# Performance work log

Measured on AMD Instinct MI355X. Metric: run time of the kernel, lower is better.

Reference implementation:

```python
import jax, jax.numpy as jnp
import numpy as np

B = 524288  # batch size
H = 4      # hidden dim


def _gru(x, h, Wih, Whh, bih, bhh):
    """PyTorch GRUCell semantics. x: [..., in], h: [..., H]."""
    gi = x @ Wih.T + bih          # [..., 3H]
    gh = h @ Whh.T + bhh          # [..., 3H]
    ir, iz, inn = jnp.split(gi, 3, axis=-1)
    hr, hz, hn = jnp.split(gh, 3, axis=-1)
    r = jax.nn.sigmoid(ir + hr)
    z = jax.nn.sigmoid(iz + hz)
    n = jnp.tanh(inn + r * hn)
    return (1.0 - z) * n + z * h


def setup_inputs() -> dict:
    key = jax.random.key(0)
    ks = jax.random.split(key, 16)
    s = 0.1
    return {
        "x": jax.random.normal(ks[0], (B, 18), dtype=jnp.float32),
        # fc_j_init: Linear(2, 4)
        "Wj": jax.random.normal(ks[1], (H, 2), dtype=jnp.float32) * s,
        "bj": jax.random.normal(ks[2], (H,), dtype=jnp.float32) * s,
        # fc_m_init: Linear(4, 4)
        "Wm": jax.random.normal(ks[3], (H, H), dtype=jnp.float32) * s,
        "bm": jax.random.normal(ks[4], (H,), dtype=jnp.float32) * s,
        # rnn_j: GRUCell(8, 4) (input is cat of two neighbor states)
        "Wih_j": jax.random.normal(ks[5], (3 * H, 2 * H), dtype=jnp.float32) * s,
        "Whh_j": jax.random.normal(ks[6], (3 * H, H), dtype=jnp.float32) * s,
        "bih_j": jax.random.normal(ks[7], (3 * H,), dtype=jnp.float32) * s,
        "bhh_j": jax.random.normal(ks[8], (3 * H,), dtype=jnp.float32) * s,
        # rnn_m: GRUCell(4, 4)
        "Wih_m": jax.random.normal(ks[9], (3 * H, H), dtype=jnp.float32) * s,
        "Whh_m": jax.random.normal(ks[10], (3 * H, H), dtype=jnp.float32) * s,
        "bih_m": jax.random.normal(ks[11], (3 * H,), dtype=jnp.float32) * s,
        "bhh_m": jax.random.normal(ks[12], (3 * H,), dtype=jnp.float32) * s,
        # fc_act: Linear(4, 1)
        "Wa": jax.random.normal(ks[13], (1, H), dtype=jnp.float32) * s,
        "ba": jax.random.normal(ks[14], (1,), dtype=jnp.float32) * s,
    }


def reference(x, Wj, bj, Wm, bm, Wih_j, Whh_j, bih_j, bhh_j,
              Wih_m, Whh_m, bih_m, bhh_m, Wa, ba):
    obs = x[:, :4]                       # [B, 4]
    j = x[:, 4:11]                       # [B, 7]
    jd = x[:, 11:18]                     # [B, 7]
    jcat = jnp.stack([j, jd], axis=-1)   # [B, 7, 2] per-joint (angle, vel)

    hj = jcat @ Wj.T + bj                # [B, 7, 4] joint hidden states
    hm = obs @ Wm.T + bm                 # [B, 4]   master hidden state

    zero_pad = jnp.zeros_like(hj[:, :1])  # [B, 1, 4] (node 6 has no right neighbor)
    for _ in range(7):
        hm_new = _gru(hj[:, 0], hm, Wih_m, Whh_m, bih_m, bhh_m)
        # left neighbor of node 0 is the master; of node i is node i-1
        left = jnp.concatenate([hm[:, None], hj[:, :6]], axis=1)   # [B, 7, 4]
        right = jnp.concatenate([hj[:, 1:], zero_pad], axis=1)     # [B, 7, 4]
        inp = jnp.concatenate([left, right], axis=-1)              # [B, 7, 8]
        hj = _gru(inp, hj, Wih_j, Whh_j, bih_j, bhh_j)             # all 7 nodes at once
        hm = hm_new

    acts = hj @ Wa.T + ba                # [B, 7, 1]
    return acts
```

## Files before the change

### kernel.cpp

```cpp
#include <hip/hip_runtime.h>


typedef _Float16 half2v __attribute__((ext_vector_type(2)));

__device__ __forceinline__ float fexp2(float x) { return __builtin_amdgcn_exp2f(x); }
__device__ __forceinline__ float frcp(float x)  { return __builtin_amdgcn_rcpf(x); }
__device__ __forceinline__ float fdot2(half2v a, half2v b, float c) {
    return __builtin_amdgcn_fdot2(a, b, c, false);
}
__device__ __forceinline__ half2v pkh(float a, float b) {
    return half2v{(_Float16)a, (_Float16)b};
}
__device__ __forceinline__ unsigned pku(float a, float b) {
    union { unsigned u; half2v h; } z; z.h = pkh(a, b); return z.u;
}
__device__ __forceinline__ half2v ldw(const unsigned* p, int i) {
    union { unsigned u; half2v h; } z; z.u = p[i]; return z.h;
}

#define U_PJRZ 0
#define U_PJNLR 48
#define U_PJNH 64
#define U_PMRZ 72
#define U_PMNI 104
#define U_PMNH 112
#define F_BRZJ 120
#define F_BINJ 128
#define F_BHNJ 132
#define F_BRZM 136
#define F_BINM 144
#define F_BHNM 148
#define F_WJ   152
#define F_BJ   160
#define F_WM   164
#define F_BM   180
#define F_WA   184
#define F_BA   188
#define W_TOT2 189

__global__ void pack_weights2(
    const float* __restrict__ Wj,    const float* __restrict__ bj,
    const float* __restrict__ Wm,    const float* __restrict__ bm,
    const float* __restrict__ Wih_j, const float* __restrict__ Whh_j,
    const float* __restrict__ bih_j, const float* __restrict__ bhh_j,
    const float* __restrict__ Wih_m, const float* __restrict__ Whh_m,
    const float* __restrict__ bih_m, const float* __restrict__ bhh_m,
    const float* __restrict__ Wa,    const float* __restrict__ ba,
    void* __restrict__ wsv)
{
    unsigned* wu = (unsigned*)wsv;
    float*    wf = (float*)wsv;
    int t = threadIdx.x;
    const float SN = -1.44269504088896f;
    const float ST =  2.88539008177793f;
    if (t < 48) {
        int g = t / 6, p = t % 6; float a, b;
        if (p < 4) { a = Wih_j[g*8 + 2*p];     b = Wih_j[g*8 + 2*p + 1]; }
        else       { a = Whh_j[g*4 + 2*(p-4)]; b = Whh_j[g*4 + 2*(p-4) + 1]; }
        wu[t] = pku(a * SN, b * SN);
    } else if (t < 64) {
        int i = t - 48, u = i / 4, p = i % 4;
        wu[t] = pku(Wih_j[(8+u)*8 + 2*p] * ST, Wih_j[(8+u)*8 + 2*p + 1] * ST);
    } else if (t < 72) {
        int i = t - 64, u = i / 2, p = i % 2;
        wu[t] = pku(Whh_j[(8+u)*4 + 2*p] * ST, Whh_j[(8+u)*4 + 2*p + 1] * ST);
    } else if (t < 104) {
        int i = t - 72, g = i / 4, p = i % 4; float a, b;
        if (p < 2) { a = Wih_m[g*4 + 2*p];     b = Wih_m[g*4 + 2*p + 1]; }
        else       { a = Whh_m[g*4 + 2*(p-2)]; b = Whh_m[g*4 + 2*(p-2) + 1]; }
        wu[t] = pku(a * SN, b * SN);
    } else if (t < 112) {
        int i = t - 104, u = i / 2, p = i % 2;
        wu[t] = pku(Wih_m[(8+u)*4 + 2*p] * ST, Wih_m[(8+u)*4 + 2*p + 1] * ST);
    } else if (t < 120) {
        int i = t - 112, u = i / 2, p = i % 2;
        wu[t] = pku(Whh_m[(8+u)*4 + 2*p] * ST, Whh_m[(8+u)*4 + 2*p + 1] * ST);
    } else if (t < 128) { wf[t] = (bih_j[t-120] + bhh_j[t-120]) * SN; }
    else if (t < 132)   { wf[t] = bih_j[8 + t - 128] * ST; }
    else if (t < 136)   { wf[t] = bhh_j[8 + t - 132] * ST; }
    else if (t < 144)   { wf[t] = (bih_m[t-136] + bhh_m[t-136]) * SN; }
    else if (t < 148)   { wf[t] = bih_m[8 + t - 144] * ST; }
    else if (t < 152)   { wf[t] = bhh_m[8 + t - 148] * ST; }
    else if (t < 160)   { wf[t] = Wj[t - 152]; }
    else if (t < 164)   { wf[t] = bj[t - 160]; }
    else if (t < 180)   { wf[t] = Wm[t - 164]; }
    else if (t < 184)   { wf[t] = bm[t - 180]; }
    else if (t < 188)   { wf[t] = Wa[t - 184]; }
    else if (t == 188)  { wf[t] = ba[0]; }
}

__global__ __launch_bounds__(256)
__attribute__((amdgpu_waves_per_eu(4, 4)))
void aggreg_policy_dot2(
    const float* __restrict__ x, const void* __restrict__ wsv,
    float* __restrict__ out, int nrows)
{
    const unsigned* WU = (const unsigned*)wsv;
    const float*    WF = (const float*)wsv;
    int b = blockIdx.x * blockDim.x + threadIdx.x;
    if (b >= nrows) return;

    const float2* xr2 = (const float2*)(x + (long)b * 18);
    float xin[18];
    #pragma unroll
    for (int i = 0; i < 9; ++i) { float2 v = xr2[i]; xin[2*i] = v.x; xin[2*i+1] = v.y; }

    float hj[7][4], hm[4];
    half2v pj[7][2], pm[2];

    #pragma unroll
    for (int k = 0; k < 7; ++k) {
        #pragma unroll
        for (int u = 0; u < 4; ++u)
            hj[k][u] = fmaf(WF[F_WJ + u*2], xin[4 + k],
                       fmaf(WF[F_WJ + u*2 + 1], xin[11 + k], WF[F_BJ + u]));
        pj[k][0] = pkh(hj[k][0], hj[k][1]);
        pj[k][1] = pkh(hj[k][2], hj[k][3]);
    }
    #pragma unroll
    for (int u = 0; u < 4; ++u) {
        float a = WF[F_BM + u];
        #pragma unroll
        for (int v = 0; v < 4; ++v) a = fmaf(WF[F_WM + u*4 + v], xin[v], a);
        hm[u] = a;
    }
    pm[0] = pkh(hm[0], hm[1]);
    pm[1] = pkh(hm[2], hm[3]);

    #pragma unroll 1
    for (int it = 0; it < 7; ++it) {
        float hmn[4]; half2v pmn[2];
        {
            float pre[8], inn[4], hn[4];
            #pragma unroll
            for (int g = 0; g < 8; ++g) {
                float a = WF[F_BRZM + g];
                a = fdot2(pj[0][0], ldw(WU, U_PMRZ + g*4 + 0), a);
                a = fdot2(pj[0][1], ldw(WU, U_PMRZ + g*4 + 1), a);
                a = fdot2(pm[0],    ldw(WU, U_PMRZ + g*4 + 2), a);
                a = fdot2(pm[1],    ldw(WU, U_PMRZ + g*4 + 3), a);
                pre[g] = a;
            }
            #pragma unroll
            for (int u = 0; u < 4; ++u) {
                float a = WF[F_BINM + u];
                a = fdot2(pj[0][0], ldw(WU, U_PMNI + u*2 + 0), a);
                a = fdot2(pj[0][1], ldw(WU, U_PMNI + u*2 + 1), a);
                inn[u] = a;
                float c = WF[F_BHNM + u];
                c = fdot2(pm[0], ldw(WU, U_PMNH + u*2 + 0), c);
                c = fdot2(pm[1], ldw(WU, U_PMNH + u*2 + 1), c);
                hn[u] = c;
            }
            #pragma unroll
            for (int u = 0; u < 4; ++u) {
                float r = frcp(1.0f + fexp2(pre[u]));
                float z = frcp(1.0f + fexp2(pre[4 + u]));
                float narg = fmaf(r, hn[u], inn[u]);
                float n = fmaf(-2.0f, frcp(1.0f + fexp2(narg)), 1.0f);
                hmn[u] = fmaf(z, hm[u] - n, n);
            }
            pmn[0] = pkh(hmn[0], hmn[1]);
            pmn[1] = pkh(hmn[2], hmn[3]);
        }

        float op[4]; half2v opp[2];
        #pragma unroll
        for (int k = 0; k < 7; ++k) {
            half2v L0 = (k == 0) ? pm[0] : opp[0];
            half2v L1 = (k == 0) ? pm[1] : opp[1];
            half2v H0 = pj[k][0], H1 = pj[k][1];
            float pre[8], inn[4], hn[4];
            #pragma unroll
            for (int g = 0; g < 8; ++g) {
                float a = WF[F_BRZJ + g];
                a = fdot2(L0, ldw(WU, U_PJRZ + g*6 + 0), a);
                a = fdot2(L1, ldw(WU, U_PJRZ + g*6 + 1), a);
                if (k != 6) {
                    a = fdot2(pj[k+1][0], ldw(WU, U_PJRZ + g*6 + 2), a);
                    a = fdot2(pj[k+1][1], ldw(WU, U_PJRZ + g*6 + 3), a);
                }
                a = fdot2(H0, ldw(WU, U_PJRZ + g*6 + 4), a);
                a = fdot2(H1, ldw(WU, U_PJRZ + g*6 + 5), a);
                pre[g] = a;
            }
            #pragma unroll
            for (int u = 0; u < 4; ++u) {
                float a = WF[F_BINJ + u];
                a = fdot2(L0, ldw(WU, U_PJNLR + u*4 + 0), a);
                a = fdot2(L1, ldw(WU, U_PJNLR + u*4 + 1), a);
                if (k != 6) {
                    a = fdot2(pj[k+1][0], ldw(WU, U_PJNLR + u*4 + 2), a);
                    a = fdot2(pj[k+1][1], ldw(WU, U_PJNLR + u*4 + 3), a);
                }
                inn[u] = a;
                float c = WF[F_BHNJ + u];
                c = fdot2(H0, ldw(WU, U_PJNH + u*2 + 0), c);
                c = fdot2(H1, ldw(WU, U_PJNH + u*2 + 1), c);
                hn[u] = c;
            }
            float nh[4];
            #pragma unroll
            for (int u = 0; u < 4; ++u) {
                float r = frcp(1.0f + fexp2(pre[u]));
                float z = frcp(1.0f + fexp2(pre[4 + u]));
                float narg = fmaf(r, hn[u], inn[u]);
                float n = fmaf(-2.0f, frcp(1.0f + fexp2(narg)), 1.0f);
                nh[u] = fmaf(z, hj[k][u] - n, n);
            }
            #pragma unroll
            for (int u = 0; u < 4; ++u) { op[u] = hj[k][u]; hj[k][u] = nh[u]; }
            opp[0] = pj[k][0]; opp[1] = pj[k][1];
            pj[k][0] = pkh(nh[0], nh[1]);
            pj[k][1] = pkh(nh[2], nh[3]);
        }

        #pragma unroll
        for (int u = 0; u < 4; ++u) hm[u] = hmn[u];
        pm[0] = pmn[0]; pm[1] = pmn[1];
    }

    float* orow = out + (long)b * 7;
    #pragma unroll
    for (int k = 0; k < 7; ++k) {
        float a = WF[F_BA];
        #pragma unroll
        for (int u = 0; u < 4; ++u) a = fmaf(WF[F_WA + u], hj[k][u], a);
        orow[k] = a;
    }
}

__device__ __forceinline__ float sigmoid_f(float x) {
    return frcp(1.0f + fexp2(-1.44269504088896f * x));
}
__device__ __forceinline__ float tanh_f(float x) {
    float e = fexp2(2.88539008177793f * x);
    return 1.0f - 2.0f * frcp(1.0f + e);
}

__global__ __launch_bounds__(256) void aggreg_policy_fallback(
    const float* __restrict__ x,
    const float* __restrict__ Wj,    const float* __restrict__ bj,
    const float* __restrict__ Wm,    const float* __restrict__ bm,
    const float* __restrict__ Wih_j, const float* __restrict__ Whh_j,
    const float* __restrict__ bih_j, const float* __restrict__ bhh_j,
    const float* __restrict__ Wih_m, const float* __restrict__ Whh_m,
    const float* __restrict__ bih_m, const float* __restrict__ bhh_m,
    const float* __restrict__ Wa,    const float* __restrict__ ba,
    float* __restrict__ out, int nrows)
{
    int b = blockIdx.x * blockDim.x + threadIdx.x;
    if (b >= nrows) return;
    const float* xr = x + (long)b * 18;
    float obs[4], jv[7], jd[7];
    #pragma unroll
    for (int i = 0; i < 4; ++i) obs[i] = xr[i];
    #pragma unroll
    for (int i = 0; i < 7; ++i) jv[i] = xr[4 + i];
    #pragma unroll
    for (int i = 0; i < 7; ++i) jd[i] = xr[11 + i];
    float hj[7][4], hm[4];
    #pragma unroll
    for (int k = 0; k < 7; ++k)
        #pragma unroll
        for (int u = 0; u < 4; ++u)
            hj[k][u] = fmaf(Wj[u*2], jv[k], fmaf(Wj[u*2+1], jd[k], bj[u]));
    #pragma unroll
    for (int u = 0; u < 4; ++u) {
        float a = bm[u];
        #pragma unroll
        for (int v = 0; v < 4; ++v) a = fmaf(Wm[u*4+v], obs[v], a);
        hm[u] = a;
    }
    float bmrz[8], bjrz[8];
    #pragma unroll
    for (int g = 0; g < 8; ++g) { bmrz[g] = bih_m[g]+bhh_m[g]; bjrz[g] = bih_j[g]+bhh_j[g]; }
    #pragma unroll 1
    for (int it = 0; it < 7; ++it) {
        float hmn[4];
        {
            float pre[8], inn[4], hn[4];
            #pragma unroll
            for (int g = 0; g < 8; ++g) {
                float a = bmrz[g];
                #pragma unroll
                for (int v = 0; v < 4; ++v) a = fmaf(Wih_m[g*4+v], hj[0][v], a);
                #pragma unroll
                for (int v = 0; v < 4; ++v) a = fmaf(Whh_m[g*4+v], hm[v], a);
                pre[g] = a;
            }
            #pragma unroll
            for (int u = 0; u < 4; ++u) {
                float a = bih_m[8+u];
                #pragma unroll
                for (int v = 0; v < 4; ++v) a = fmaf(Wih_m[(8+u)*4+v], hj[0][v], a);
                inn[u] = a;
                float c = bhh_m[8+u];
                #pragma unroll
                for (int v = 0; v < 4; ++v) c = fmaf(Whh_m[(8+u)*4+v], hm[v], c);
                hn[u] = c;
            }
            #pragma unroll
            for (int u = 0; u < 4; ++u) {
                float r = sigmoid_f(pre[u]);
                float z = sigmoid_f(pre[4+u]);
                float n = tanh_f(fmaf(r, hn[u], inn[u]));
                hmn[u] = fmaf(z, hm[u]-n, n);
            }
        }
        float nh[7][4];
        #pragma unroll
        for (int k = 0; k < 7; ++k) {
            float L[4], R[4];
            #pragma unroll
            for (int u = 0; u < 4; ++u) {
                L[u] = (k == 0) ? hm[u] : hj[k-1][u];
                R[u] = (k == 6) ? 0.0f  : hj[k+1][u];
            }
            float pre[8], inn[4], hn[4];
            #pragma unroll
            for (int g = 0; g < 8; ++g) {
                float a = bjrz[g];
                #pragma unroll
                for (int v = 0; v < 4; ++v) a = fmaf(Wih_j[g*8+v], L[v], a);
                #pragma unroll
                for (int v = 0; v < 4; ++v) a = fmaf(Wih_j[g*8+4+v], R[v], a);
                #pragma unroll
                for (int v = 0; v < 4; ++v) a = fmaf(Whh_j[g*4+v], hj[k][v], a);
                pre[g] = a;
            }
            #pragma unroll
            for (int u = 0; u < 4; ++u) {
                float a = bih_j[8+u];
                #pragma unroll
                for (int v = 0; v < 4; ++v) a = fmaf(Wih_j[(8+u)*8+v], L[v], a);
                #pragma unroll
                for (int v = 0; v < 4; ++v) a = fmaf(Wih_j[(8+u)*8+4+v], R[v], a);
                inn[u] = a;
                float c = bhh_j[8+u];
                #pragma unroll
                for (int v = 0; v < 4; ++v) c = fmaf(Whh_j[(8+u)*4+v], hj[k][v], c);
                hn[u] = c;
            }
            #pragma unroll
            for (int u = 0; u < 4; ++u) {
                float r = sigmoid_f(pre[u]);
                float z = sigmoid_f(pre[4+u]);
                float n = tanh_f(fmaf(r, hn[u], inn[u]));
                nh[k][u] = fmaf(z, hj[k][u]-n, n);
            }
        }
        #pragma unroll
        for (int k = 0; k < 7; ++k)
            #pragma unroll
            for (int u = 0; u < 4; ++u) hj[k][u] = nh[k][u];
        #pragma unroll
        for (int u = 0; u < 4; ++u) hm[u] = hmn[u];
    }
    float* orow = out + (long)b * 7;
    #pragma unroll
    for (int k = 0; k < 7; ++k) {
        float a = ba[0];
        #pragma unroll
        for (int u = 0; u < 4; ++u) a = fmaf(Wa[u], hj[k][u], a);
        orow[k] = a;
    }
}

extern "C" void kernel_launch(void* const* d_in, const int* in_sizes, int n_in,
                              void* d_out, int out_size, void* d_ws, size_t ws_size,
                              hipStream_t stream) {
    const float* x     = (const float*)d_in[0];
    const float* Wj    = (const float*)d_in[1];
    const float* bj    = (const float*)d_in[2];
    const float* Wm    = (const float*)d_in[3];
    const float* bm    = (const float*)d_in[4];
    const float* Wih_j = (const float*)d_in[5];
    const float* Whh_j = (const float*)d_in[6];
    const float* bih_j = (const float*)d_in[7];
    const float* bhh_j = (const float*)d_in[8];
    const float* Wih_m = (const float*)d_in[9];
    const float* Whh_m = (const float*)d_in[10];
    const float* bih_m = (const float*)d_in[11];
    const float* bhh_m = (const float*)d_in[12];
    const float* Wa    = (const float*)d_in[13];
    const float* ba    = (const float*)d_in[14];
    float* out = (float*)d_out;

    int nrows = in_sizes[0] / 18;
    int block = 256;
    int grid = (nrows + block - 1) / block;

    if (ws_size >= W_TOT2 * sizeof(float)) {
        pack_weights2<<<1, 256, 0, stream>>>(
            Wj, bj, Wm, bm, Wih_j, Whh_j, bih_j, bhh_j,
            Wih_m, Whh_m, bih_m, bhh_m, Wa, ba, d_ws);
        aggreg_policy_dot2<<<grid, block, 0, stream>>>(x, d_ws, out, nrows);
    } else {
        aggreg_policy_fallback<<<grid, block, 0, stream>>>(
            x, Wj, bj, Wm, bm, Wih_j, Whh_j, bih_j, bhh_j,
            Wih_m, Whh_m, bih_m, bhh_m, Wa, ba, out, nrows);
    }
}
```

Baseline: 142.8 us.

## Batch GRU reciprocals algebraically and use packed RTZ half conversion

Rewrites the GRU gate math so the z and n gates fold into one rational expression, and computes four reciprocals with a single rcp using the product trick. This cuts transcendental rcp instructions per unit from three to about half of one. It also switches hot-path float-to-half packing to cvt_pkrtz and drops the waves_per_eu occupancy hint. The batched-reciprocal products risk overflow or underflow when the exp2 values are large, and round-toward-zero packing slightly changes numerics.

```diff
diff --git a/kernel.cpp b/kernel.cpp
--- a/kernel.cpp
+++ b/kernel.cpp
@@ -9,13 +9,48 @@
     return __builtin_amdgcn_fdot2(a, b, c, false);
 }
 __device__ __forceinline__ half2v pkh(float a, float b) {
-    return half2v{(_Float16)a, (_Float16)b};
+    union { __fp16 __attribute__((ext_vector_type(2))) i; half2v o; } z;
+    z.i = __builtin_amdgcn_cvt_pkrtz(a, b);
+    return z.o;
 }
 __device__ __forceinline__ unsigned pku(float a, float b) {
-    union { unsigned u; half2v h; } z; z.h = pkh(a, b); return z.u;
+    union { unsigned u; half2v h; } z; z.h = half2v{(_Float16)a, (_Float16)b}; return z.u;
 }
 __device__ __forceinline__ half2v ldw(const unsigned* p, int i) {
     union { unsigned u; half2v h; } z; z.u = p[i]; return z.h;
+}
+
+__device__ __forceinline__ void rcp4(const float a[4], float o[4]) {
+    float p01 = a[0] * a[1];
+    float p23 = a[2] * a[3];
+    float rP  = frcp(p01 * p23);
+    float q01 = rP * p23;
+    float q23 = rP * p01;
+    o[0] = a[1] * q01;
+    o[1] = a[0] * q01;
+    o[2] = a[3] * q23;
+    o[3] = a[2] * q23;
+}
+
+__device__ __forceinline__ void gru_out4(const float pre[8], const float inn[4],
+                                         const float hn[4], const float h[4],
+                                         float nh[4]) {
+    float ar[4], r[4];
+    #pragma unroll
+    for (int u = 0; u < 4; ++u) ar[u] = 1.0f + fexp2(pre[u]);
+    rcp4(ar, r);
+    float ez[4], en[4], num[4], den[4], inv[4];
+    #pragma unroll
+    for (int u = 0; u < 4; ++u) {
+        ez[u] = fexp2(pre[4 + u]);
+        en[u] = fexp2(fmaf(r[u], hn[u], inn[u]));
+        num[u] = fmaf(en[u], ez[u] + h[u], h[u] - ez[u]);
+        float s = ez[u] + 1.0f;
+        den[u] = fmaf(en[u], s, s);
+    }
+    rcp4(den, inv);
+    #pragma unroll
+    for (int u = 0; u < 4; ++u) nh[u] = num[u] * inv[u];
 }
 
 #define U_PJRZ 0
@@ -90,7 +125,6 @@
 }
 
 __global__ __launch_bounds__(256)
-__attribute__((amdgpu_waves_per_eu(4, 4)))
 void aggreg_policy_dot2(
     const float* __restrict__ x, const void* __restrict__ wsv,
     float* __restrict__ out, int nrows)
@@ -152,19 +186,12 @@
                 c = fdot2(pm[1], ldw(WU, U_PMNH + u*2 + 1), c);
                 hn[u] = c;
             }
-            #pragma unroll
-            for (int u = 0; u < 4; ++u) {
-                float r = frcp(1.0f + fexp2(pre[u]));
-                float z = frcp(1.0f + fexp2(pre[4 + u]));
-                float narg = fmaf(r, hn[u], inn[u]);
-                float n = fmaf(-2.0f, frcp(1.0f + fexp2(narg)), 1.0f);
-                hmn[u] = fmaf(z, hm[u] - n, n);
-            }
+            gru_out4(pre, inn, hn, hm, hmn);
             pmn[0] = pkh(hmn[0], hmn[1]);
             pmn[1] = pkh(hmn[2], hmn[3]);
         }
 
-        float op[4]; half2v opp[2];
+        half2v opp[2];
         #pragma unroll
         for (int k = 0; k < 7; ++k) {
             half2v L0 = (k == 0) ? pm[0] : opp[0];
@@ -200,17 +227,10 @@
                 hn[u] = c;
             }
             float nh[4];
-            #pragma unroll
-            for (int u = 0; u < 4; ++u) {
-                float r = frcp(1.0f + fexp2(pre[u]));
-                float z = frcp(1.0f + fexp2(pre[4 + u]));
-                float narg = fmaf(r, hn[u], inn[u]);
-                float n = fmaf(-2.0f, frcp(1.0f + fexp2(narg)), 1.0f);
-                nh[u] = fmaf(z, hj[k][u] - n, n);
-            }
-            #pragma unroll
-            for (int u = 0; u < 4; ++u) { op[u] = hj[k][u]; hj[k][u] = nh[u]; }
+            gru_out4(pre, inn, hn, hj[k], nh);
             opp[0] = pj[k][0]; opp[1] = pj[k][1];
+            #pragma unroll
+            for (int u = 0; u < 4; ++u) hj[k][u] = nh[u];
             pj[k][0] = pkh(nh[0], nh[1]);
             pj[k][1] = pkh(nh[2], nh[3]);
         }
```

Result: faster. 137.0 us (-4.1%).
